# Performance work log

Measured on AMD Instinct MI355X. Metric: run time of the kernel, lower is better.

## Reference

```python
import jax, jax.numpy as jnp
import numpy as np

N_TOKEN = 267735
D_EMBED = 1024
D_PROJ = 1024
DIV_VAL = 4
CUTOFF_ENDS = [0, 20000, 40000, 200000, N_TOKEN]
EMB_SCALE = D_PROJ ** 0.5
INIT_STD = 0.02


def setup_inputs() -> dict:
    key = jax.random.key(0)
    ks = jax.random.split(key, 9)
    inp = jax.random.randint(ks[0], (4, 4096), 0, N_TOKEN, dtype=jnp.int32)
    out = {"inp": inp}
    for i in range(4):
        l, r = CUTOFF_ENDS[i], CUTOFF_ENDS[i + 1]
        d_i = D_EMBED // DIV_VAL ** i  # 1024, 256, 64, 16
        tbl = jax.random.normal(ks[1 + i], (r - l, d_i), dtype=jnp.float32)
        # padding_idx=1: row 1 is zero-initialized in torch nn.Embedding
        tbl = tbl.at[1].set(0.0)
        out[f"emb{i}"] = tbl
        out[f"proj{i}"] = jax.random.normal(ks[5 + i], (D_PROJ, d_i), dtype=jnp.float32) * INIT_STD
    return out


def reference(inp, emb0, emb1, emb2, emb3, proj0, proj1, proj2, proj3):
    tables = [emb0, emb1, emb2, emb3]
    projs = [proj0, proj1, proj2, proj3]
    flat = inp.reshape(-1)                                  # [N]
    out = jnp.zeros((flat.shape[0], D_PROJ), dtype=emb0.dtype)
    for i in range(4):
        l, r = CUTOFF_ENDS[i], CUTOFF_ENDS[i + 1]
        mask = (flat >= l) & (flat < r)                     # [N] bool
        local = jnp.clip(flat - l, 0, r - l - 1)            # in-range local idx
        e_i = tables[i][local]                              # [N, d_i] gather
        p_i = jnp.einsum('nd,pd->np', e_i, projs[i])        # [N, D_PROJ]
        out = out + jnp.where(mask[:, None], p_i, 0.0)      # scatter-by-mask
    out = out * EMB_SCALE
    return out.reshape(*inp.shape, D_PROJ)
```

## Files before the change

### kernel.cpp

```cpp
#include <hip/hip_runtime.h>
#include <hip/hip_bf16.h>

#define DPROJ 1024

typedef float  f32x4  __attribute__((ext_vector_type(4)));
typedef short  bf16x8 __attribute__((ext_vector_type(8)));

__device__ __forceinline__ unsigned pk2(float a, float b) {
    __hip_bfloat162 h = __float22bfloat162_rn(make_float2(a, b));
    unsigned r; __builtin_memcpy(&r, &h, 4); return r;
}

__device__ __forceinline__ void gll16(const void* g, void* l) {
    __builtin_amdgcn_global_load_lds(
        (const __attribute__((address_space(1))) void*)g,
        (__attribute__((address_space(3))) void*)l, 16, 0, 0);
}

__global__ __launch_bounds__(256) void k_prep(
    const int* __restrict__ inp, int n,
    int* __restrict__ cnt, int* __restrict__ lists,
    const float* __restrict__ p0, const float* __restrict__ p1,
    const float* __restrict__ p2, const float* __restrict__ p3,
    short* __restrict__ pb0, short* __restrict__ pb1,
    short* __restrict__ pb2, short* __restrict__ pb3)
{
    const int tid = threadIdx.x;
    const int b   = blockIdx.x;
    const int CB  = (n + 255) >> 8;
    if (b < CB) {
        const int t = b * 256 + tid;
        int c = -1, l = 0;
        if (t < n) {
            const int x = inp[t];
            c = (x >= 20000) + (x >= 40000) + (x >= 200000);
            l = x - ((c == 0) ? 0 : (c == 1) ? 20000 : (c == 2) ? 40000 : 200000);
        }
        const int lane = tid & 63;
        int pos = 0;
        #pragma unroll
        for (int cc = 0; cc < 4; ++cc) {
            const unsigned long long mk = __ballot(c == cc);
            if (c == cc) {
                const int lead = __ffsll(mk) - 1;
                int base = 0;
                if (lane == lead) base = atomicAdd(&cnt[cc], (int)__popcll(mk));
                base = __shfl(base, lead);
                pos  = base + (int)__popcll(mk & ((1ull << lane) - 1ull));
            }
        }
        if (t < n) lists[c * n + pos] = (int)(((unsigned)t << 18) | (unsigned)l);
    } else {
        const long g = (long)(b - CB) * 256 + tid;
        const float* src; short* dst; long lo;
        if      (g < 131072) { src = p0; dst = pb0; lo = g; }
        else if (g < 163840) { src = p1; dst = pb1; lo = g - 131072; }
        else if (g < 172032) { src = p2; dst = pb2; lo = g - 163840; }
        else if (g < 174080) { src = p3; dst = pb3; lo = g - 172032; }
        else return;
        const float4 a = *(const float4*)(src + lo * 8);
        const float4 c4 = *(const float4*)(src + lo * 8 + 4);
        uint4 q; q.x = pk2(a.x, a.y);   q.y = pk2(a.z, a.w);
                 q.z = pk2(c4.x, c4.y); q.w = pk2(c4.z, c4.w);
        *(uint4*)(dst + lo * 8) = q;
    }
}

__global__ __launch_bounds__(256, 4) void k_gemm(
    const int* __restrict__ cnt, const int* __restrict__ lists, int n,
    const float* __restrict__ e0, const float* __restrict__ e1,
    const float* __restrict__ e2, const float* __restrict__ e3,
    const short* __restrict__ pb0, const short* __restrict__ pb1,
    const short* __restrict__ pb2, const short* __restrict__ pb3,
    float* __restrict__ out)
{
    constexpr int TM = 64, TN = 128, KC = 32, ESTR = 40;

    const int z     = blockIdx.z;
    const int count = cnt[z];
    const int row0  = blockIdx.y * TM;
    if (row0 >= count) return;

    const float* emb = (z == 0) ? e0  : (z == 1) ? e1  : (z == 2) ? e2  : e3;
    const short* pb  = (z == 0) ? pb0 : (z == 1) ? pb1 : (z == 2) ? pb2 : pb3;
    const int    K   = (z == 0) ? 1024 : (z == 1) ? 256 : (z == 2) ? 64 : 16;
    const int*  list = lists + (size_t)z * n;
    const int   col0 = blockIdx.x * TN;

    __shared__ int   s_tok[TM];
    __shared__ int   s_loc[TM];
    __shared__ short e_s[2][TM * ESTR];
    __shared__ short p_s[2][4 * TN * 8];

    const int tid = threadIdx.x;
    if (tid < TM) {
        int r = row0 + tid;
        if (r < count) {
            unsigned pk = (unsigned)list[r];
            s_tok[tid] = (int)(pk >> 18);
            s_loc[tid] = (int)(pk & 0x3FFFFu);
        } else { s_tok[tid] = -1; s_loc[tid] = -1; }
    }
    __syncthreads();

    const int wave = tid >> 6, lane = tid & 63;
    const int lm = lane & 15, quad = lane >> 4;

    const int erow = tid >> 2, egrp = tid & 3;
    const int eloc = s_loc[erow];
    const bool ev  = (eloc >= 0);
    const float* ebase = emb + (ev ? (size_t)eloc * K : 0) + egrp * 8;
    const int eoff = erow * ESTR + egrp * 8;
    short* ebuf = (short*)e_s;
    short* pbuf = (short*)p_s;

    const short* pg0 = pb + (size_t)(col0 +      lane) * K + wave * 8;
    const short* pg1 = pb + (size_t)(col0 + 64 + lane) * K + wave * 8;
    const int pdoff0 = wave * 128 * 8;
    const int pdoff1 = wave * 128 * 8 + 64 * 8;

    f32x4 acc[8];
    #pragma unroll
    for (int i = 0; i < 8; ++i) acc[i] = (f32x4){0.f, 0.f, 0.f, 0.f};

    const int nt = (K + KC - 1) / KC;
    float ef[8];

    {
        const bool v = ev && (egrp * 8 < K);
        if (v) {
            float4 a = *(const float4*)(ebase);
            float4 b = *(const float4*)(ebase + 4);
            ef[0] = a.x; ef[1] = a.y; ef[2] = a.z; ef[3] = a.w;
            ef[4] = b.x; ef[5] = b.y; ef[6] = b.z; ef[7] = b.w;
        } else {
            #pragma unroll
            for (int j = 0; j < 8; ++j) ef[j] = 0.f;
        }
        gll16(pg0, pbuf + pdoff0);
        gll16(pg1, pbuf + pdoff1);
        uint4 q; q.x = pk2(ef[0], ef[1]); q.y = pk2(ef[2], ef[3]);
                 q.z = pk2(ef[4], ef[5]); q.w = pk2(ef[6], ef[7]);
        *(uint4*)(ebuf + eoff) = q;
    }
    __syncthreads();

    for (int t = 0; t < nt; ++t) {
        const int  cur = t & 1;
        const int  kn  = (t + 1) * KC;
        const bool pf  = (kn < K);
        if (pf) {
            const bool v = ev && (kn + egrp * 8 < K);
            if (v) {
                const float* s = ebase + kn;
                float4 a = *(const float4*)(s);
                float4 b = *(const float4*)(s + 4);
                ef[0] = a.x; ef[1] = a.y; ef[2] = a.z; ef[3] = a.w;
                ef[4] = b.x; ef[5] = b.y; ef[6] = b.z; ef[7] = b.w;
            } else {
                #pragma unroll
                for (int j = 0; j < 8; ++j) ef[j] = 0.f;
            }
            const int nb = (cur ^ 1) * 4096;
            gll16(pg0 + kn, pbuf + nb + pdoff0);
            gll16(pg1 + kn, pbuf + nb + pdoff1);
        }

        bf16x8 ebf = *(const bf16x8*)(ebuf + cur * (TM * ESTR)
                                      + (wave * 16 + lm) * ESTR + quad * 8);
        const short* pk_ = pbuf + cur * 4096 + quad * (TN * 8) + lm * 8;
        #pragma unroll
        for (int ns = 0; ns < 8; ++ns) {
            bf16x8 pfr = *(const bf16x8*)(pk_ + ns * 128);
            acc[ns] = __builtin_amdgcn_mfma_f32_16x16x32_bf16(pfr, ebf, acc[ns], 0, 0, 0);
        }

        if (pf) {
            uint4 q; q.x = pk2(ef[0], ef[1]); q.y = pk2(ef[2], ef[3]);
                     q.z = pk2(ef[4], ef[5]); q.w = pk2(ef[6], ef[7]);
            *(uint4*)(ebuf + (cur ^ 1) * (TM * ESTR) + eoff) = q;
        }
        __syncthreads();
    }

    const int tok = s_tok[wave * 16 + lm];
    if (tok >= 0) {
        float* orow = out + (size_t)tok * DPROJ + col0 + quad * 4;
        #pragma unroll
        for (int ns = 0; ns < 8; ++ns) {
            f32x4 v = acc[ns] * 32.f;
            __builtin_nontemporal_store(v, (f32x4*)(orow + ns * 16));
        }
    }
}

extern "C" void kernel_launch(void* const* d_in, const int* in_sizes, int n_in,
                              void* d_out, int out_size, void* d_ws, size_t ws_size,
                              hipStream_t stream) {
    const int*   inp = (const int*)d_in[0];
    const float* e0  = (const float*)d_in[1];
    const float* p0  = (const float*)d_in[2];
    const float* e1  = (const float*)d_in[3];
    const float* p1  = (const float*)d_in[4];
    const float* e2  = (const float*)d_in[5];
    const float* p2  = (const float*)d_in[6];
    const float* e3  = (const float*)d_in[7];
    const float* p3  = (const float*)d_in[8];
    float* out = (float*)d_out;
    const int n = in_sizes[0];

    char* wsb  = (char*)d_ws;
    int* cnt   = (int*)wsb;
    int* lists = (int*)(wsb + 16);
    size_t off = 16 + (size_t)4 * n * sizeof(int);
    off = (off + 255) & ~(size_t)255;
    short* pb0 = (short*)(wsb + off); off += (size_t)1024 * 1024 * 2;
    short* pb1 = (short*)(wsb + off); off += (size_t)1024 * 256 * 2;
    short* pb3 = (short*)(wsb + off); off += (size_t)1024 * 16 * 2;
    short* pb2 = (short*)(wsb + off); off += (size_t)1024 * 64 * 2;

    hipMemsetAsync(cnt, 0, 4 * sizeof(int), stream);

    const int CB = (n + 255) >> 8;
    k_prep<<<CB + 680, 256, 0, stream>>>(inp, n, cnt, lists,
                                         p0, p1, p2, p3, pb0, pb1, pb2, pb3);

    dim3 grid(DPROJ / 128, (n + 63) / 64, 4);
    k_gemm<<<grid, 256, 0, stream>>>(cnt, lists, n, e0, e1, e2, e3,
                                     pb0, pb1, pb2, pb3, out);
}
```

Baseline: 234.5 us.

## Pre-gather embeddings into compact swizzled bf16 buffer before GEMM

Adds a separate gather kernel that converts the selected embedding rows to bf16 and packs them contiguously per cluster, with an XOR swizzle and K padded to 32 for the smallest cluster. The GEMM then streams both operands via global_load_lds double buffering instead of converting fp32 in registers. The grid is reordered so row blocks come first, occupancy hint raised, and nontemporal output stores replaced by normal stores. In exchange it adds an extra kernel launch and a round trip of the gathered activations through global memory.

```diff
diff --git a/kernel.cpp b/kernel.cpp
--- a/kernel.cpp
+++ b/kernel.cpp
@@ -52,133 +52,145 @@
         if (t < n) lists[c * n + pos] = (int)(((unsigned)t << 18) | (unsigned)l);
     } else {
         const long g = (long)(b - CB) * 256 + tid;
-        const float* src; short* dst; long lo;
-        if      (g < 131072) { src = p0; dst = pb0; lo = g; }
-        else if (g < 163840) { src = p1; dst = pb1; lo = g - 131072; }
-        else if (g < 172032) { src = p2; dst = pb2; lo = g - 163840; }
-        else if (g < 174080) { src = p3; dst = pb3; lo = g - 172032; }
-        else return;
-        const float4 a = *(const float4*)(src + lo * 8);
-        const float4 c4 = *(const float4*)(src + lo * 8 + 4);
-        uint4 q; q.x = pk2(a.x, a.y);   q.y = pk2(a.z, a.w);
-                 q.z = pk2(c4.x, c4.y); q.w = pk2(c4.z, c4.w);
-        *(uint4*)(dst + lo * 8) = q;
-    }
-}
-
-__global__ __launch_bounds__(256, 4) void k_gemm(
+        if (g < 172032) {
+            const float* src; short* dst; long lo;
+            if      (g < 131072) { src = p0; dst = pb0; lo = g; }
+            else if (g < 163840) { src = p1; dst = pb1; lo = g - 131072; }
+            else                 { src = p2; dst = pb2; lo = g - 163840; }
+            const float4 a = *(const float4*)(src + lo * 8);
+            const float4 d = *(const float4*)(src + lo * 8 + 4);
+            uint4 q; q.x = pk2(a.x, a.y); q.y = pk2(a.z, a.w);
+                     q.z = pk2(d.x, d.y); q.w = pk2(d.z, d.w);
+            *(uint4*)(dst + lo * 8) = q;
+        } else if (g < 176128) {
+            const long lo = g - 172032;
+            const int col = (int)(lo >> 2), c = (int)(lo & 3);
+            uint4 q = (uint4){0u, 0u, 0u, 0u};
+            if (c < 2) {
+                const float* src = p3 + (size_t)col * 16 + c * 8;
+                const float4 a = *(const float4*)src;
+                const float4 d = *(const float4*)(src + 4);
+                q.x = pk2(a.x, a.y); q.y = pk2(a.z, a.w);
+                q.z = pk2(d.x, d.y); q.w = pk2(d.z, d.w);
+            }
+            *(uint4*)(pb3 + (size_t)col * 32 + c * 8) = q;
+        }
+    }
+}
+
+__global__ __launch_bounds__(256) void k_egather(
     const int* __restrict__ cnt, const int* __restrict__ lists, int n,
     const float* __restrict__ e0, const float* __restrict__ e1,
     const float* __restrict__ e2, const float* __restrict__ e3,
+    short* __restrict__ ec)
+{
+    const int c0 = cnt[0], c1 = cnt[1], c2 = cnt[2], c3 = cnt[3];
+    const long t0 = (long)c0 * 128;
+    const long t1 = t0 + (long)c1 * 32;
+    const long t2 = t1 + (long)c2 * 8;
+    const long t3 = t2 + (long)c3 * 4;
+    const long o1 = (long)c0 * 1024;
+    const long o2 = o1 + (long)c1 * 256;
+    const long o3 = o2 + (long)c2 * 64;
+
+    const long stride = (long)gridDim.x * 256;
+    for (long i = (long)blockIdx.x * 256 + threadIdx.x; i < t3; i += stride) {
+        int z, Kp, Kr, lc; long rem, off; const float* emb;
+        if (i < t0)      { z = 0; rem = i;      off = 0;  emb = e0; Kp = 1024; Kr = 1024; lc = 7; }
+        else if (i < t1) { z = 1; rem = i - t0; off = o1; emb = e1; Kp = 256;  Kr = 256;  lc = 5; }
+        else if (i < t2) { z = 2; rem = i - t1; off = o2; emb = e2; Kp = 64;   Kr = 64;   lc = 3; }
+        else             { z = 3; rem = i - t2; off = o3; emb = e3; Kp = 32;   Kr = 16;   lc = 2; }
+        const int r = (int)(rem >> lc);
+        const int c = (int)(rem & ((1 << lc) - 1));
+        const int k = c * 8;
+        uint4 q = (uint4){0u, 0u, 0u, 0u};
+        if (k < Kr) {
+            const int loc = lists[z * n + r] & 0x3FFFF;
+            const float* src = emb + (size_t)loc * Kr + k;
+            const float4 a = *(const float4*)src;
+            const float4 d = *(const float4*)(src + 4);
+            q.x = pk2(a.x, a.y); q.y = pk2(a.z, a.w);
+            q.z = pk2(d.x, d.y); q.w = pk2(d.z, d.w);
+        }
+        const int gsw = (c & ~3) | ((c ^ ((r >> 1) & 3)) & 3);
+        *(uint4*)(ec + off + (size_t)r * Kp + gsw * 8) = q;
+    }
+}
+
+__global__ __launch_bounds__(256, 6) void k_gemm(
+    const int* __restrict__ cnt, const int* __restrict__ lists, int n,
+    const short* __restrict__ ec,
     const short* __restrict__ pb0, const short* __restrict__ pb1,
     const short* __restrict__ pb2, const short* __restrict__ pb3,
     float* __restrict__ out)
 {
-    constexpr int TM = 64, TN = 128, KC = 32, ESTR = 40;
-
-    const int z     = blockIdx.z;
+    const int yb = blockIdx.x, z = blockIdx.y, xb = blockIdx.z;
     const int count = cnt[z];
-    const int row0  = blockIdx.y * TM;
+    const int row0  = yb * 64;
     if (row0 >= count) return;
 
-    const float* emb = (z == 0) ? e0  : (z == 1) ? e1  : (z == 2) ? e2  : e3;
-    const short* pb  = (z == 0) ? pb0 : (z == 1) ? pb1 : (z == 2) ? pb2 : pb3;
-    const int    K   = (z == 0) ? 1024 : (z == 1) ? 256 : (z == 2) ? 64 : 16;
-    const int*  list = lists + (size_t)z * n;
-    const int   col0 = blockIdx.x * TN;
-
-    __shared__ int   s_tok[TM];
-    __shared__ int   s_loc[TM];
-    __shared__ short e_s[2][TM * ESTR];
-    __shared__ short p_s[2][4 * TN * 8];
+    const int c0 = cnt[0], c1 = cnt[1], c2 = cnt[2];
+    const short* pb = (z == 0) ? pb0 : (z == 1) ? pb1 : (z == 2) ? pb2 : pb3;
+    const int    Kp = (z == 0) ? 1024 : (z == 1) ? 256 : (z == 2) ? 64 : 32;
+    const long eoff = (z == 0) ? 0
+                    : (z == 1) ? (long)c0 * 1024
+                    : (z == 2) ? (long)c0 * 1024 + (long)c1 * 256
+                               : (long)c0 * 1024 + (long)c1 * 256 + (long)c2 * 64;
+    const short* ecz  = ec + eoff;
+    const int    nt   = Kp >> 5;
+    const int    col0 = xb * 128;
+    const int*   list = lists + (size_t)z * n;
+
+    __shared__ int   s_tok[64];
+    __shared__ short e_s[2][64 * 32];
+    __shared__ short p_s[2][4 * 128 * 8];
 
     const int tid = threadIdx.x;
-    if (tid < TM) {
-        int r = row0 + tid;
-        if (r < count) {
-            unsigned pk = (unsigned)list[r];
-            s_tok[tid] = (int)(pk >> 18);
-            s_loc[tid] = (int)(pk & 0x3FFFFu);
-        } else { s_tok[tid] = -1; s_loc[tid] = -1; }
-    }
-    __syncthreads();
+    if (tid < 64) {
+        const int r = row0 + tid;
+        s_tok[tid] = (r < count) ? (int)((unsigned)list[r] >> 18) : -1;
+    }
 
     const int wave = tid >> 6, lane = tid & 63;
     const int lm = lane & 15, quad = lane >> 4;
 
-    const int erow = tid >> 2, egrp = tid & 3;
-    const int eloc = s_loc[erow];
-    const bool ev  = (eloc >= 0);
-    const float* ebase = emb + (ev ? (size_t)eloc * K : 0) + egrp * 8;
-    const int eoff = erow * ESTR + egrp * 8;
-    short* ebuf = (short*)e_s;
-    short* pbuf = (short*)p_s;
-
-    const short* pg0 = pb + (size_t)(col0 +      lane) * K + wave * 8;
-    const short* pg1 = pb + (size_t)(col0 + 64 + lane) * K + wave * 8;
-    const int pdoff0 = wave * 128 * 8;
-    const int pdoff1 = wave * 128 * 8 + 64 * 8;
+    const short* esrc = ecz + (size_t)(row0 + wave * 16 + (lane >> 2)) * Kp
+                            + (lane & 3) * 8;
+    short* eb   = &e_s[0][0];
+    const int edst = wave * 512;
+
+    const short* psrc0 = pb + (size_t)(col0 +      lane) * Kp + wave * 8;
+    const short* psrc1 = pb + (size_t)(col0 + 64 + lane) * Kp + wave * 8;
+    short* pbuf_ = &p_s[0][0];
+    const int pdst = wave * 1024;
+
+    const int eread = (wave * 16 + lm) * 32 + (quad ^ ((lm >> 1) & 3)) * 8;
+    const int pread = quad * 1024 + lm * 8;
 
     f32x4 acc[8];
     #pragma unroll
     for (int i = 0; i < 8; ++i) acc[i] = (f32x4){0.f, 0.f, 0.f, 0.f};
 
-    const int nt = (K + KC - 1) / KC;
-    float ef[8];
-
-    {
-        const bool v = ev && (egrp * 8 < K);
-        if (v) {
-            float4 a = *(const float4*)(ebase);
-            float4 b = *(const float4*)(ebase + 4);
-            ef[0] = a.x; ef[1] = a.y; ef[2] = a.z; ef[3] = a.w;
-            ef[4] = b.x; ef[5] = b.y; ef[6] = b.z; ef[7] = b.w;
-        } else {
-            #pragma unroll
-            for (int j = 0; j < 8; ++j) ef[j] = 0.f;
-        }
-        gll16(pg0, pbuf + pdoff0);
-        gll16(pg1, pbuf + pdoff1);
-        uint4 q; q.x = pk2(ef[0], ef[1]); q.y = pk2(ef[2], ef[3]);
-                 q.z = pk2(ef[4], ef[5]); q.w = pk2(ef[6], ef[7]);
-        *(uint4*)(ebuf + eoff) = q;
-    }
+    gll16(esrc,  eb    + edst);
+    gll16(psrc0, pbuf_ + pdst);
+    gll16(psrc1, pbuf_ + pdst + 512);
     __syncthreads();
 
     for (int t = 0; t < nt; ++t) {
-        const int  cur = t & 1;
-        const int  kn  = (t + 1) * KC;
-        const bool pf  = (kn < K);
-        if (pf) {
-            const bool v = ev && (kn + egrp * 8 < K);
-            if (v) {
-                const float* s = ebase + kn;
-                float4 a = *(const float4*)(s);
-                float4 b = *(const float4*)(s + 4);
-                ef[0] = a.x; ef[1] = a.y; ef[2] = a.z; ef[3] = a.w;
-                ef[4] = b.x; ef[5] = b.y; ef[6] = b.z; ef[7] = b.w;
-            } else {
-                #pragma unroll
-                for (int j = 0; j < 8; ++j) ef[j] = 0.f;
-            }
-            const int nb = (cur ^ 1) * 4096;
-            gll16(pg0 + kn, pbuf + nb + pdoff0);
-            gll16(pg1 + kn, pbuf + nb + pdoff1);
-        }
-
-        bf16x8 ebf = *(const bf16x8*)(ebuf + cur * (TM * ESTR)
-                                      + (wave * 16 + lm) * ESTR + quad * 8);
-        const short* pk_ = pbuf + cur * 4096 + quad * (TN * 8) + lm * 8;
+        const int cur = t & 1;
+        if (t + 1 < nt) {
+            const int kb = (t + 1) * 32;
+            const int nb = cur ^ 1;
+            gll16(esrc  + kb, eb    + nb * 2048 + edst);
+            gll16(psrc0 + kb, pbuf_ + nb * 4096 + pdst);
+            gll16(psrc1 + kb, pbuf_ + nb * 4096 + pdst + 512);
+        }
+        const bf16x8 ebf = *(const bf16x8*)(eb + cur * 2048 + eread);
+        const short* pk_ = pbuf_ + cur * 4096 + pread;
         #pragma unroll
         for (int ns = 0; ns < 8; ++ns) {
             bf16x8 pfr = *(const bf16x8*)(pk_ + ns * 128);
             acc[ns] = __builtin_amdgcn_mfma_f32_16x16x32_bf16(pfr, ebf, acc[ns], 0, 0, 0);
-        }
-
-        if (pf) {
-            uint4 q; q.x = pk2(ef[0], ef[1]); q.y = pk2(ef[2], ef[3]);
-                     q.z = pk2(ef[4], ef[5]); q.w = pk2(ef[6], ef[7]);
-            *(uint4*)(ebuf + (cur ^ 1) * (TM * ESTR) + eoff) = q;
         }
         __syncthreads();
     }
@@ -189,7 +201,7 @@
         #pragma unroll
         for (int ns = 0; ns < 8; ++ns) {
             f32x4 v = acc[ns] * 32.f;
-            __builtin_nontemporal_store(v, (f32x4*)(orow + ns * 16));
+            *(f32x4*)(orow + ns * 16) = v;
         }
     }
 }
@@ -216,16 +228,18 @@
     off = (off + 255) & ~(size_t)255;
     short* pb0 = (short*)(wsb + off); off += (size_t)1024 * 1024 * 2;
     short* pb1 = (short*)(wsb + off); off += (size_t)1024 * 256 * 2;
-    short* pb3 = (short*)(wsb + off); off += (size_t)1024 * 16 * 2;
     short* pb2 = (short*)(wsb + off); off += (size_t)1024 * 64 * 2;
+    short* pb3 = (short*)(wsb + off); off += (size_t)1024 * 32 * 2;
+    short* ec  = (short*)(wsb + off);
 
     hipMemsetAsync(cnt, 0, 4 * sizeof(int), stream);
 
     const int CB = (n + 255) >> 8;
-    k_prep<<<CB + 680, 256, 0, stream>>>(inp, n, cnt, lists,
+    k_prep<<<CB + 688, 256, 0, stream>>>(inp, n, cnt, lists,
                                          p0, p1, p2, p3, pb0, pb1, pb2, pb3);
-
-    dim3 grid(DPROJ / 128, (n + 63) / 64, 4);
-    k_gemm<<<grid, 256, 0, stream>>>(cnt, lists, n, e0, e1, e2, e3,
+    k_egather<<<1024, 256, 0, stream>>>(cnt, lists, n, e0, e1, e2, e3, ec);
+
+    dim3 grid((n + 63) / 64, 4, 8);
+    k_gemm<<<grid, 256, 0, stream>>>(cnt, lists, n, ec,
                                      pb0, pb1, pb2, pb3, out);
 }
```

After: 228.5 us. 1.03x faster.
